# Kernel tuning notes

Measured on AMD Instinct MI355X. Metric: run time of the kernel, lower is better.

## Reference

```python
import jax, jax.numpy as jnp
import numpy as np

D = 1024            # text/user embedding length
HID = 3 * D         # 2*text_D + user_D = MLP hidden width
OUT = 8             # output_shape (int)


def setup_inputs() -> dict:
    key = jax.random.key(0)
    ks = jax.random.split(key, 9)
    T, U = 256, 128
    s = 1.0 / np.sqrt(HID)
    return {
        "text_a": jax.random.normal(ks[0], (T, D), jnp.float32),
        "text_b": jax.random.normal(ks[1], (T, D), jnp.float32),
        "user_embeddings": jax.random.normal(ks[2], (U, D), jnp.float32),
        "W1": jax.random.uniform(ks[3], (HID, HID), jnp.float32, -s, s),
        "b1": jax.random.uniform(ks[4], (HID,), jnp.float32, -s, s),
        "W2": jax.random.uniform(ks[5], (HID, HID), jnp.float32, -s, s),
        "b2": jax.random.uniform(ks[6], (HID,), jnp.float32, -s, s),
        "W3": jax.random.uniform(ks[7], (OUT, HID), jnp.float32, -s, s),
        "b3": jax.random.uniform(ks[8], (OUT,), jnp.float32, -s, s),
    }


def reference(text_a, text_b, user_embeddings, W1, b1, W2, b2, W3, b3):
    # min/max over the set of text embedding tensors
    t_min = jnp.minimum(text_a, text_b)          # (T, D)
    t_max = jnp.maximum(text_a, text_b)          # (T, D)
    T, U = t_min.shape[0], user_embeddings.shape[0]
    # combined[t, u] = concat(t_min[t], t_max[t], user[u])  -> (T, U, 3D)
    text_part = jnp.broadcast_to(
        jnp.concatenate([t_min, t_max], axis=-1)[:, None, :], (T, U, 2 * D))
    user_part = jnp.broadcast_to(user_embeddings[None, :, :], (T, U, D))
    x = jnp.concatenate([text_part, user_part], axis=-1)  # (T, U, 3D)
    # 3-layer MLP (no activation, no dropout by default)
    x = jnp.einsum('tuh,oh->tuo', x, W1) + b1
    x = jnp.einsum('tuh,oh->tuo', x, W2) + b2
    x = jnp.einsum('tuh,oh->tuo', x, W3) + b3
    return x  # (T, U, OUT)
```

## Files before the change

kernel.cpp:

```cpp
#include <hip/hip_runtime.h>
#include <hip/hip_bf16.h>


#define HIDN 3072
#define DIM 1024
#define NOUT 8
#define NS 32
#define KPS 96
#define RPT 12
#define GX 24
#define CPB 128
#define TDIM 256
#define UDIM 128
#define PF4 6144

__device__ __forceinline__ float4 f4z() { return make_float4(0.f, 0.f, 0.f, 0.f); }
__device__ __forceinline__ float4 add4(float4 a, float4 b) {
    return make_float4(a.x + b.x, a.y + b.y, a.z + b.z, a.w + b.w);
}
__device__ __forceinline__ float dot4(float4 a, float4 b) {
    return a.x * b.x + a.y * b.y + a.z * b.z + a.w * b.w;
}

__device__ __forceinline__ void bias_slice_fold(const float* As,
                                                const float* __restrict__ bvec,
                                                float* __restrict__ cp,
                                                int s, int tid) {
    const int o = tid >> 5, k5 = tid & 31;
    float acc = 0.f;
#pragma unroll
    for (int j = 0; j < KPS / 32; ++j)
        acc += As[o * KPS + k5 + 32 * j] * bvec[s * KPS + k5 + 32 * j];
#pragma unroll
    for (int off = 16; off; off >>= 1) acc += __shfl_down(acc, off, 32);
    if (k5 == 0) cp[s * NOUT + o] = acc;
}

__global__ __launch_bounds__(256) void gemm_partial(
    const float* __restrict__ A_rows, const float* __restrict__ part_in,
    const float* __restrict__ B, float* __restrict__ part_out,
    const float* __restrict__ bvec, float* __restrict__ cp, int mode) {
    const int s = blockIdx.y, gx = blockIdx.x;
    const int tid = threadIdx.x;
    const int rq = tid >> 5, c4 = tid & 31;

    __shared__ float As[NOUT * KPS];
    __shared__ float4 red[8 * NOUT * 32];

    if (mode == 0) {
        for (int i = tid; i < NOUT * KPS; i += 256)
            As[i] = A_rows[(i / KPS) * HIDN + s * KPS + (i % KPS)];
    } else {
        if (tid < NOUT * KPS / 4) {
            const int j4 = tid;
            const int o = j4 / (KPS / 4), kk4 = j4 % (KPS / 4);
            const float4* pp = (const float4*)(part_in + (size_t)o * HIDN
                                               + s * KPS) + kk4;
            float4 a = f4z();
#pragma unroll 8
            for (int sp = 0; sp < NS; ++sp)
                a = add4(a, pp[(size_t)sp * PF4]);
            ((float4*)As)[j4] = a;
        }
    }
    __syncthreads();
    if (gx == 0) bias_slice_fold(As, bvec, cp, s, tid);

    const int k0 = s * KPS + rq * RPT;
    const float4* Bp = (const float4*)(B + (size_t)k0 * HIDN) + gx * 32 + c4;

    float4 bv[RPT];
#pragma unroll
    for (int kk = 0; kk < RPT; ++kk) bv[kk] = Bp[(size_t)kk * (HIDN / 4)];

    float4 acc[NOUT];
#pragma unroll
    for (int o = 0; o < NOUT; ++o) acc[o] = f4z();
#pragma unroll
    for (int kk = 0; kk < RPT; ++kk) {
#pragma unroll
        for (int o = 0; o < NOUT; ++o) {
            float a = As[o * KPS + rq * RPT + kk];
            acc[o].x += a * bv[kk].x; acc[o].y += a * bv[kk].y;
            acc[o].z += a * bv[kk].z; acc[o].w += a * bv[kk].w;
        }
    }

#pragma unroll
    for (int o = 0; o < NOUT; ++o) red[rq * 256 + o * 32 + c4] = acc[o];
    __syncthreads();
    {
        const int o = tid >> 5, cc = tid & 31;
        float4 r = f4z();
#pragma unroll
        for (int q = 0; q < 8; ++q) r = add4(r, red[q * 256 + o * 32 + cc]);
        *(float4*)(part_out + ((size_t)s * NOUT + o) * HIDN + gx * CPB + cc * 4) = r;
    }
}

__global__ __launch_bounds__(256) void k3_mid(
    const float* __restrict__ part2, const float* __restrict__ user,
    const float* __restrict__ cp1, const float* __restrict__ cp2,
    const float* __restrict__ b3, float* __restrict__ Mt,
    float* __restrict__ Qpart, float* __restrict__ cvec) {
    const int b = blockIdx.x, tid = threadIdx.x;
    const float4* p4 = (const float4*)part2;

    if (b < 64) {
        const int lane = tid & 63, w = tid >> 6;
        const int i4 = b * 64 + lane;
        const int o = i4 >> 9, h4 = i4 & 511;
        float4 acc = f4z();
#pragma unroll
        for (int j = 0; j < 8; ++j)
            acc = add4(acc, p4[(size_t)(w * 8 + j) * PF4 + o * 768 + h4]);
        __shared__ float4 red2[4 * 64];
        red2[w * 64 + lane] = acc;
        __syncthreads();
        if (w == 0) {
            float4 r = add4(add4(red2[lane], red2[64 + lane]),
                            add4(red2[128 + lane], red2[192 + lane]));
            ((float4*)Mt)[i4] = r;
        }
        return;
    }

    if (b < 96) {
        const int ub = b - 64;
        __shared__ float4 mup[4 * 64];
        __shared__ float4 Mu4[NOUT * 8];
        const int tgt = tid & 63, grp = tid >> 6;
        const int o = tgt >> 3, j4 = tgt & 7;
        float4 a = f4z();
#pragma unroll
        for (int j = 0; j < 8; ++j)
            a = add4(a, p4[(size_t)(grp * 8 + j) * PF4 + o * 768 + 512 + ub * 8 + j4]);
        mup[grp * 64 + tgt] = a;
        __syncthreads();
        if (tid < 64)
            Mu4[tid] = add4(add4(mup[tid], mup[64 + tid]),
                            add4(mup[128 + tid], mup[192 + tid]));
        __syncthreads();

        const int u = tid >> 1, o0 = (tid & 1) * 4;
        const float4* uv = (const float4*)user + (size_t)u * (DIM / 4) + ub * 8;
        float4 x8[8];
#pragma unroll
        for (int j = 0; j < 8; ++j) x8[j] = uv[j];
        float q[4];
#pragma unroll
        for (int oo = 0; oo < 4; ++oo) {
            float s = 0.f;
#pragma unroll
            for (int j = 0; j < 8; ++j) s += dot4(Mu4[(o0 + oo) * 8 + j], x8[j]);
            q[oo] = s;
        }
        ((float4*)Qpart)[((size_t)ub * UDIM + u) * 2 + (tid & 1)] =
            make_float4(q[0], q[1], q[2], q[3]);
        return;
    }

    if (tid < NOUT) {
        float cc = b3[tid];
#pragma unroll 8
        for (int s = 0; s < NS; ++s)
            cc += cp1[s * NOUT + tid] + cp2[s * NOUT + tid];
        cvec[tid] = cc;
    }
}

__global__ __launch_bounds__(256) void k4_out(
    const float* __restrict__ ta, const float* __restrict__ tb,
    const float* __restrict__ Mt, const float* __restrict__ Qpart,
    const float* __restrict__ cvec, float4* __restrict__ out) {
    const int t = blockIdx.x, tid = threadIdx.x;
    const int lane = tid & 63, w = tid >> 6;

    const float4* Mt4 = (const float4*)Mt;
    float4 a = ((const float4*)ta)[(size_t)t * (DIM / 4) + tid];
    float4 b = ((const float4*)tb)[(size_t)t * (DIM / 4) + tid];
    float4 mn = make_float4(fminf(a.x, b.x), fminf(a.y, b.y),
                            fminf(a.z, b.z), fminf(a.w, b.w));
    float4 mx = make_float4(fmaxf(a.x, b.x), fmaxf(a.y, b.y),
                            fmaxf(a.z, b.z), fmaxf(a.w, b.w));
    float acc[NOUT];
#pragma unroll
    for (int o = 0; o < NOUT; ++o) {
        float4 ml = Mt4[o * 512 + tid];
        float4 mh = Mt4[o * 512 + 256 + tid];
        acc[o] = dot4(ml, mn) + dot4(mh, mx);
    }
#pragma unroll
    for (int o = 0; o < NOUT; ++o) {
#pragma unroll
        for (int off = 32; off > 0; off >>= 1)
            acc[o] += __shfl_down(acc[o], off, 64);
    }
    __shared__ float red[4][NOUT];
    if (lane == 0) {
#pragma unroll
        for (int o = 0; o < NOUT; ++o) red[w][o] = acc[o];
    }
    __syncthreads();

    const int u = tid >> 1, half = tid & 1, o0 = half * 4;
    const float4* Qp4 = (const float4*)Qpart;
    float4 q = f4z();
#pragma unroll 8
    for (int ub = 0; ub < 32; ++ub)
        q = add4(q, Qp4[((size_t)ub * UDIM + u) * 2 + half]);

    float4 cv = ((const float4*)cvec)[half];
    float4 pv = make_float4(
        red[0][o0 + 0] + red[1][o0 + 0] + red[2][o0 + 0] + red[3][o0 + 0],
        red[0][o0 + 1] + red[1][o0 + 1] + red[2][o0 + 1] + red[3][o0 + 1],
        red[0][o0 + 2] + red[1][o0 + 2] + red[2][o0 + 2] + red[3][o0 + 2],
        red[0][o0 + 3] + red[1][o0 + 3] + red[2][o0 + 3] + red[3][o0 + 3]);
    out[(size_t)t * 256 + tid] = add4(add4(pv, q), cv);
}

extern "C" void kernel_launch(void* const* d_in, const int* in_sizes, int n_in,
                              void* d_out, int out_size, void* d_ws, size_t ws_size,
                              hipStream_t stream) {
    const float* text_a = (const float*)d_in[0];
    const float* text_b = (const float*)d_in[1];
    const float* user   = (const float*)d_in[2];
    const float* W1 = (const float*)d_in[3];
    const float* b1 = (const float*)d_in[4];
    const float* W2 = (const float*)d_in[5];
    const float* b2 = (const float*)d_in[6];
    const float* W3 = (const float*)d_in[7];
    const float* b3 = (const float*)d_in[8];

    float* ws = (float*)d_ws;
    float* part1 = ws;
    float* part2 = part1 + (size_t)NS * NOUT * HIDN;
    float* Mt    = part2 + (size_t)NS * NOUT * HIDN;
    float* Qpart = Mt + NOUT * 2048;
    float* cp1   = Qpart + 32 * UDIM * NOUT;
    float* cp2   = cp1 + NS * NOUT;
    float* cvec  = cp2 + NS * NOUT;

    gemm_partial<<<dim3(GX, NS), 256, 0, stream>>>(W3, nullptr, W2, part1,
                                                   b2, cp2, 0);
    gemm_partial<<<dim3(GX, NS), 256, 0, stream>>>(nullptr, part1, W1, part2,
                                                   b1, cp1, 1);
    k3_mid<<<97, 256, 0, stream>>>(part2, user, cp1, cp2, b3, Mt, Qpart, cvec);
    k4_out<<<TDIM, 256, 0, stream>>>(text_a, text_b, Mt, Qpart, cvec,
                                     (float4*)d_out);
}
```

Baseline: 33.01 us.

## Hoist W loads before partial reduction, widen k3 Mt reduction, fold bias into k4

In gemm_partial, the per-thread loads of the B-matrix rows are issued before the A-slice load and partial-sum reduction, so that weight-streaming latency overlaps the reduction and the barrier. The partial-sum unroll rises from 8 to 16. k3_mid splits the Mt reduction across 128 blocks of 32 outputs with 8 groups, instead of 64 blocks with 4 groups, for more parallelism. The separate bias-vector block is removed and each k4_out block recomputes the bias constant itself. The hoisted loads raise register pressure, and k4 repeats a small redundant reduction in every block.

```diff
diff --git a/kernel.cpp b/kernel.cpp
--- a/kernel.cpp
+++ b/kernel.cpp
@@ -47,6 +47,12 @@
     __shared__ float As[NOUT * KPS];
     __shared__ float4 red[8 * NOUT * 32];
 
+    const int k0 = s * KPS + rq * RPT;
+    const float4* Bp = (const float4*)(B + (size_t)k0 * HIDN) + gx * 32 + c4;
+    float4 bv[RPT];
+#pragma unroll
+    for (int kk = 0; kk < RPT; ++kk) bv[kk] = Bp[(size_t)kk * (HIDN / 4)];
+
     if (mode == 0) {
         for (int i = tid; i < NOUT * KPS; i += 256)
             As[i] = A_rows[(i / KPS) * HIDN + s * KPS + (i % KPS)];
@@ -57,7 +63,7 @@
             const float4* pp = (const float4*)(part_in + (size_t)o * HIDN
                                                + s * KPS) + kk4;
             float4 a = f4z();
-#pragma unroll 8
+#pragma unroll 16
             for (int sp = 0; sp < NS; ++sp)
                 a = add4(a, pp[(size_t)sp * PF4]);
             ((float4*)As)[j4] = a;
@@ -65,13 +71,6 @@
     }
     __syncthreads();
     if (gx == 0) bias_slice_fold(As, bvec, cp, s, tid);
-
-    const int k0 = s * KPS + rq * RPT;
-    const float4* Bp = (const float4*)(B + (size_t)k0 * HIDN) + gx * 32 + c4;
-
-    float4 bv[RPT];
-#pragma unroll
-    for (int kk = 0; kk < RPT; ++kk) bv[kk] = Bp[(size_t)kk * (HIDN / 4)];
 
     float4 acc[NOUT];
 #pragma unroll
@@ -100,79 +99,69 @@
 
 __global__ __launch_bounds__(256) void k3_mid(
     const float* __restrict__ part2, const float* __restrict__ user,
-    const float* __restrict__ cp1, const float* __restrict__ cp2,
-    const float* __restrict__ b3, float* __restrict__ Mt,
-    float* __restrict__ Qpart, float* __restrict__ cvec) {
+    float* __restrict__ Mt, float* __restrict__ Qpart) {
     const int b = blockIdx.x, tid = threadIdx.x;
     const float4* p4 = (const float4*)part2;
 
-    if (b < 64) {
-        const int lane = tid & 63, w = tid >> 6;
-        const int i4 = b * 64 + lane;
+    if (b < 128) {
+        const int li = tid & 31, sg = tid >> 5;
+        const int i4 = b * 32 + li;
         const int o = i4 >> 9, h4 = i4 & 511;
         float4 acc = f4z();
 #pragma unroll
-        for (int j = 0; j < 8; ++j)
-            acc = add4(acc, p4[(size_t)(w * 8 + j) * PF4 + o * 768 + h4]);
-        __shared__ float4 red2[4 * 64];
-        red2[w * 64 + lane] = acc;
+        for (int j = 0; j < 4; ++j)
+            acc = add4(acc, p4[(size_t)(sg * 4 + j) * PF4 + o * 768 + h4]);
+        __shared__ float4 red2[8 * 32];
+        red2[sg * 32 + li] = acc;
         __syncthreads();
-        if (w == 0) {
-            float4 r = add4(add4(red2[lane], red2[64 + lane]),
-                            add4(red2[128 + lane], red2[192 + lane]));
-            ((float4*)Mt)[i4] = r;
+        if (tid < 32) {
+            const int i4w = b * 32 + tid;
+            float4 r = f4z();
+#pragma unroll
+            for (int q = 0; q < 8; ++q) r = add4(r, red2[q * 32 + tid]);
+            ((float4*)Mt)[i4w] = r;
         }
         return;
     }
 
-    if (b < 96) {
-        const int ub = b - 64;
-        __shared__ float4 mup[4 * 64];
-        __shared__ float4 Mu4[NOUT * 8];
-        const int tgt = tid & 63, grp = tid >> 6;
-        const int o = tgt >> 3, j4 = tgt & 7;
-        float4 a = f4z();
-#pragma unroll
-        for (int j = 0; j < 8; ++j)
-            a = add4(a, p4[(size_t)(grp * 8 + j) * PF4 + o * 768 + 512 + ub * 8 + j4]);
-        mup[grp * 64 + tgt] = a;
-        __syncthreads();
-        if (tid < 64)
-            Mu4[tid] = add4(add4(mup[tid], mup[64 + tid]),
-                            add4(mup[128 + tid], mup[192 + tid]));
-        __syncthreads();
-
-        const int u = tid >> 1, o0 = (tid & 1) * 4;
-        const float4* uv = (const float4*)user + (size_t)u * (DIM / 4) + ub * 8;
-        float4 x8[8];
-#pragma unroll
-        for (int j = 0; j < 8; ++j) x8[j] = uv[j];
-        float q[4];
-#pragma unroll
-        for (int oo = 0; oo < 4; ++oo) {
-            float s = 0.f;
-#pragma unroll
-            for (int j = 0; j < 8; ++j) s += dot4(Mu4[(o0 + oo) * 8 + j], x8[j]);
-            q[oo] = s;
-        }
-        ((float4*)Qpart)[((size_t)ub * UDIM + u) * 2 + (tid & 1)] =
-            make_float4(q[0], q[1], q[2], q[3]);
-        return;
-    }
-
-    if (tid < NOUT) {
-        float cc = b3[tid];
-#pragma unroll 8
-        for (int s = 0; s < NS; ++s)
-            cc += cp1[s * NOUT + tid] + cp2[s * NOUT + tid];
-        cvec[tid] = cc;
-    }
+    const int ub = b - 128;
+    __shared__ float4 mup[4 * 64];
+    __shared__ float4 Mu4[NOUT * 8];
+    const int tgt = tid & 63, grp = tid >> 6;
+    const int o = tgt >> 3, j4 = tgt & 7;
+    float4 a = f4z();
+#pragma unroll
+    for (int j = 0; j < 8; ++j)
+        a = add4(a, p4[(size_t)(grp * 8 + j) * PF4 + o * 768 + 512 + ub * 8 + j4]);
+    mup[grp * 64 + tgt] = a;
+    __syncthreads();
+    if (tid < 64)
+        Mu4[tid] = add4(add4(mup[tid], mup[64 + tid]),
+                        add4(mup[128 + tid], mup[192 + tid]));
+    __syncthreads();
+
+    const int u = tid >> 1, o0 = (tid & 1) * 4;
+    const float4* uv = (const float4*)user + (size_t)u * (DIM / 4) + ub * 8;
+    float4 x8[8];
+#pragma unroll
+    for (int j = 0; j < 8; ++j) x8[j] = uv[j];
+    float q[4];
+#pragma unroll
+    for (int oo = 0; oo < 4; ++oo) {
+        float s = 0.f;
+#pragma unroll
+        for (int j = 0; j < 8; ++j) s += dot4(Mu4[(o0 + oo) * 8 + j], x8[j]);
+        q[oo] = s;
+    }
+    ((float4*)Qpart)[((size_t)ub * UDIM + u) * 2 + (tid & 1)] =
+        make_float4(q[0], q[1], q[2], q[3]);
 }
 
 __global__ __launch_bounds__(256) void k4_out(
     const float* __restrict__ ta, const float* __restrict__ tb,
     const float* __restrict__ Mt, const float* __restrict__ Qpart,
-    const float* __restrict__ cvec, float4* __restrict__ out) {
+    const float* __restrict__ cp1, const float* __restrict__ cp2,
+    const float* __restrict__ b3, float4* __restrict__ out) {
     const int t = blockIdx.x, tid = threadIdx.x;
     const int lane = tid & 63, w = tid >> 6;
 
@@ -197,9 +186,17 @@
             acc[o] += __shfl_down(acc[o], off, 64);
     }
     __shared__ float red[4][NOUT];
+    __shared__ float c8[NOUT];
     if (lane == 0) {
 #pragma unroll
         for (int o = 0; o < NOUT; ++o) red[w][o] = acc[o];
+    }
+    if (tid < NOUT) {
+        float cc = b3[tid];
+#pragma unroll 8
+        for (int s = 0; s < NS; ++s)
+            cc += cp1[s * NOUT + tid] + cp2[s * NOUT + tid];
+        c8[tid] = cc;
     }
     __syncthreads();
 
@@ -210,7 +207,7 @@
     for (int ub = 0; ub < 32; ++ub)
         q = add4(q, Qp4[((size_t)ub * UDIM + u) * 2 + half]);
 
-    float4 cv = ((const float4*)cvec)[half];
+    float4 cv = make_float4(c8[o0], c8[o0 + 1], c8[o0 + 2], c8[o0 + 3]);
     float4 pv = make_float4(
         red[0][o0 + 0] + red[1][o0 + 0] + red[2][o0 + 0] + red[3][o0 + 0],
         red[0][o0 + 1] + red[1][o0 + 1] + red[2][o0 + 1] + red[3][o0 + 1],
@@ -239,13 +236,12 @@
     float* Qpart = Mt + NOUT * 2048;
     float* cp1   = Qpart + 32 * UDIM * NOUT;
     float* cp2   = cp1 + NS * NOUT;
-    float* cvec  = cp2 + NS * NOUT;
 
     gemm_partial<<<dim3(GX, NS), 256, 0, stream>>>(W3, nullptr, W2, part1,
                                                    b2, cp2, 0);
     gemm_partial<<<dim3(GX, NS), 256, 0, stream>>>(nullptr, part1, W1, part2,
                                                    b1, cp1, 1);
-    k3_mid<<<97, 256, 0, stream>>>(part2, user, cp1, cp2, b3, Mt, Qpart, cvec);
-    k4_out<<<TDIM, 256, 0, stream>>>(text_a, text_b, Mt, Qpart, cvec,
+    k3_mid<<<160, 256, 0, stream>>>(part2, user, Mt, Qpart);
+    k4_out<<<TDIM, 256, 0, stream>>>(text_a, text_b, Mt, Qpart, cp1, cp2, b3,
                                      (float4*)d_out);
 }
```

Measured after the change: 36.40 us. 10.3% more time.
